# Kernel tuning notes

Hardware: AMD Instinct MI355X
Metric: run time of the kernel (lower is better)

The kernel has to match this reference:

```python
import jax, jax.numpy as jnp
from jax import lax
import numpy as np

NUM_CLASSES = 10
NUM_ITERS = 3


def conv2d(x, w, stride):
    return lax.conv_general_dilated(x, w, window_strides=stride, padding='VALID',
                                    dimension_numbers=('NCHW', 'OIHW', 'NCHW'))


def deconv(x, w_torch, stride, pad):
    # w_torch: [Cin, Cout, k, k] (PyTorch ConvTranspose2d layout)
    k = w_torch.shape[2]
    w = jnp.flip(w_torch, axis=(2, 3)).transpose(1, 0, 2, 3)  # -> [Cout, Cin, k, k]
    return lax.conv_general_dilated(x, w, window_strides=(1, 1),
                                    padding=[(k - 1 - pad, k - 1 - pad)] * 2,
                                    lhs_dilation=(stride, stride),
                                    dimension_numbers=('NCHW', 'OIHW', 'NCHW'))


def squash(t, axis=-1):
    sq = jnp.sum(t * t, axis=axis, keepdims=True)
    return (sq / (1.0 + sq)) * t / jnp.sqrt(sq)


def batchnorm(t, g, b, eps=1e-5):
    # training-mode batch statistics over (N, H, W)
    m = t.mean(axis=(0, 2, 3), keepdims=True)
    v = t.var(axis=(0, 2, 3), keepdims=True)
    return g[None, :, None, None] * (t - m) / jnp.sqrt(v + eps) + b[None, :, None, None]


def setup_inputs() -> dict:
    key = jax.random.key(0)
    ks = jax.random.split(key, 16)
    B = 128
    d = dict(
        x=jax.random.normal(ks[0], (B, 3, 32, 32), jnp.float32),
        conv1_w=jax.random.normal(ks[1], (256, 3, 9, 9), jnp.float32) * 0.05,
        conv1_b=jnp.zeros((256,), jnp.float32),
        prim_w=jax.random.normal(ks[2], (8, 64, 256, 9, 9), jnp.float32) * 0.02,
        prim_b=jnp.zeros((8, 64), jnp.float32),
        route_w=jax.random.normal(ks[3], (NUM_CLASSES, 4096, 8, 16), jnp.float32),
        g1_w=jax.random.normal(ks[4], (160, 256, 4, 4), jnp.float32) * 0.02,
        g2_w=jax.random.normal(ks[5], (256, 128, 4, 4), jnp.float32) * 0.02,
        g3_w=jax.random.normal(ks[6], (128, 64, 4, 4), jnp.float32) * 0.02,
        g4_w=jax.random.normal(ks[7], (64, 3, 4, 4), jnp.float32) * 0.02,
        bn1_g=jnp.ones((256,), jnp.float32), bn1_b=jnp.zeros((256,), jnp.float32),
        bn2_g=jnp.ones((128,), jnp.float32), bn2_b=jnp.zeros((128,), jnp.float32),
        bn3_g=jnp.ones((64,), jnp.float32), bn3_b=jnp.zeros((64,), jnp.float32),
    )
    return d


def reference(x, conv1_w, conv1_b, prim_w, prim_b, route_w,
              g1_w, g2_w, g3_w, g4_w,
              bn1_g, bn1_b, bn2_g, bn2_b, bn3_g, bn3_b):
    B = x.shape[0]
    # conv stem: [B,3,32,32] -> [B,256,24,24]
    h = jax.nn.relu(conv2d(x, conv1_w, (1, 1)) + conv1_b[None, :, None, None])
    # primary capsules: 8 parallel convs fused into one [8*64,256,9,9] conv -> [B,512,8,8]
    u = conv2d(h, prim_w.reshape(8 * 64, 256, 9, 9), (2, 2)) + prim_b.reshape(8 * 64)[None, :, None, None]
    # cat over capsules on last dim: route node = flat (c,h,w) per capsule -> [B,4096,8]
    u = u.reshape(B, 8, 64 * 8 * 8).transpose(0, 2, 1)
    u = squash(u, axis=-1)
    # digit capsules: priors [C,B,R,16]
    priors = jnp.einsum('bri,crio->cbro', u, route_w)
    logits = jnp.zeros(priors.shape[:3], priors.dtype)  # [C,B,R]
    v = None
    for i in range(NUM_ITERS):
        probs = jax.nn.softmax(logits, axis=2)  # over route nodes (dim=2 in original)
        v = squash(jnp.einsum('cbr,cbro->cbo', probs, priors), axis=-1)  # [C,B,16]
        if i != NUM_ITERS - 1:
            logits = logits + jnp.einsum('cbro,cbo->cbr', priors, v)
    caps = v.transpose(1, 0, 2)  # [B,10,16]
    classes = jax.nn.softmax(jnp.sqrt(jnp.sum(caps * caps, axis=-1)), axis=-1)  # [B,10]
    # y = one-hot of predicted class (inference path, y=None)
    y = jax.nn.one_hot(jnp.argmax(classes, axis=1), NUM_CLASSES, dtype=caps.dtype)
    z = (caps * y[:, :, None]).reshape(B, 160, 1, 1)
    # DCGAN generator: 1 -> 4 -> 8 -> 16 -> 32
    t = jax.nn.relu(batchnorm(deconv(z, g1_w, 1, 0), bn1_g, bn1_b))
    t = jax.nn.relu(batchnorm(deconv(t, g2_w, 2, 1), bn2_g, bn2_b))
    t = jax.nn.relu(batchnorm(deconv(t, g3_w, 2, 1), bn3_g, bn3_b))
    recon = jnp.tanh(deconv(t, g4_w, 2, 1))  # [B,3,32,32]
    return classes, recon
```

## Files before the change

kernel.cpp:

```cpp
#include <hip/hip_runtime.h>
#include <cmath>

#define NB 128

#define H_STRIDE 600
#define W_SLAB   7776

__global__ __launch_bounds__(192) void conv1_kernel(
    const float* __restrict__ x, const float* __restrict__ w,
    const float* __restrict__ bias, float* __restrict__ h)
{
    __shared__ float4 xs4[768];
    float* xs = (float*)xs4;
    int b = blockIdx.x, cobase = blockIdx.y * 8, tid = threadIdx.x;
    const float4* xsrc = (const float4*)(x + (size_t)b * 3072);
    for (int i = tid; i < 768; i += 192) xs4[i] = xsrc[i];
    __syncthreads();
    for (int round = 0; round < 3; ++round) {
        int px = round * 192 + tid;
        int yy = px / 24, xx = px - yy * 24;
        float acc[8];
        #pragma unroll
        for (int cc = 0; cc < 8; ++cc) acc[cc] = 0.f;
        for (int c = 0; c < 3; ++c)
            for (int ky = 0; ky < 9; ++ky) {
                const float* xr = xs + c * 1024 + (yy + ky) * 32 + xx;
                float xv[9];
                #pragma unroll
                for (int kx = 0; kx < 9; ++kx) xv[kx] = xr[kx];
                int tb = c * 81 + ky * 9;
                #pragma unroll
                for (int cc = 0; cc < 8; ++cc) {
                    const float* wp = w + (cobase + cc) * 243 + tb;
                    #pragma unroll
                    for (int kx = 0; kx < 9; ++kx) acc[cc] += xv[kx] * wp[kx];
                }
            }
        #pragma unroll
        for (int cc = 0; cc < 8; ++cc)
            h[((size_t)b * 256 + cobase + cc) * H_STRIDE + yy * 25 + xx] =
                fmaxf(acc[cc] + bias[cobase + cc], 0.f);
    }
}

__global__ __launch_bounds__(128) void primw_transpose_kernel(
    const float* __restrict__ pw, float* __restrict__ wt)
{
    int g = blockIdx.x >> 8, ci = blockIdx.x & 255;
    int half = threadIdx.x >> 6, lane = threadIdx.x & 63;
    for (int ch = half; ch < 64; ch += 2) {
        int oct = ch >> 3, k = ch & 7;
        const float* src = pw + ((size_t)(g * 64 + ch) * 256 + ci) * 81;
        float* dst = wt + (size_t)(g * 256 + ci) * W_SLAB + oct * 12 + k;
        dst[(size_t)lane * 96] = src[lane];
        if (lane < 17) dst[(size_t)(64 + lane) * 96] = src[64 + lane];
    }
}

__global__ __launch_bounds__(256) void prim_conv_kernel(
    const float* __restrict__ h, const float* __restrict__ wt,
    float* __restrict__ part)
{
    __shared__ __align__(16) float wsh[W_SLAB];
    __shared__ __align__(16) float hsh[2 * H_STRIDE];
    int b2 = blockIdx.x, g = blockIdx.y, half = blockIdx.z, tid = threadIdx.x;
    int ci0 = half * 128;
    int img = tid >> 7;
    int t128 = tid & 127;
    int oct = t128 & 7;
    int pq = t128 >> 3;
    int px0 = pq * 4;
    int y0 = pq >> 1, x0 = (pq & 1) * 4;
    int b = b2 * 2 + img;
    int hbase = img * H_STRIDE;

    float acc[8][4];
    #pragma unroll
    for (int i = 0; i < 8; ++i)
        #pragma unroll
        for (int j = 0; j < 4; ++j) acc[i][j] = 0.f;

    #define STAGE(ci)                                                                        \
    {                                                                                        \
        const float* wsrc = wt + (size_t)(g * 256 + (ci)) * W_SLAB;                          \
        const float* h0src = h + ((size_t)(b2 * 2 + 0) * 256 + (ci)) * H_STRIDE;             \
        const float* h1src = h + ((size_t)(b2 * 2 + 1) * 256 + (ci)) * H_STRIDE;             \
        _Pragma("unroll")                                                                    \
        for (int k = 0; k < 7; ++k)                                                          \
            __builtin_amdgcn_global_load_lds(                                                \
                (const unsigned int*)wsrc + (k * 256 + tid) * 4,                             \
                (unsigned int*)wsh + (k * 256 + tid) * 4, 16, 0, 0);                         \
        if (tid < 152)                                                                       \
            __builtin_amdgcn_global_load_lds(                                                \
                (const unsigned int*)wsrc + (1792 + tid) * 4,                                \
                (unsigned int*)wsh + (1792 + tid) * 4, 16, 0, 0);                            \
        if (tid < 150)                                                                       \
            __builtin_amdgcn_global_load_lds(                                                \
                (const unsigned int*)h0src + tid * 4,                                        \
                (unsigned int*)hsh + tid * 4, 16, 0, 0);                                     \
        if (tid < 150)                                                                       \
            __builtin_amdgcn_global_load_lds(                                                \
                (const unsigned int*)h1src + tid * 4,                                        \
                (unsigned int*)(hsh + H_STRIDE) + tid * 4, 16, 0, 0);                        \
    }

    STAGE(ci0);
    asm volatile("s_waitcnt vmcnt(0)" ::: "memory");
    __syncthreads();

    for (int ci = ci0; ci < ci0 + 128; ++ci) {
        #pragma unroll 3
        for (int ky = 0; ky < 9; ++ky) {
            int hrowbase = hbase + (2 * y0 + ky) * 25 + 2 * x0;
            #pragma unroll
            for (int kx = 0; kx < 9; ++kx) {
                const float* wp = wsh + (ky * 9 + kx) * 96 + oct * 12;
                float4 wa = *(const float4*)(wp);
                float4 wb = *(const float4*)(wp + 4);
                int hr = hrowbase + kx;
                float h0 = hsh[hr];
                float h1 = hsh[hr + 2];
                float h2 = hsh[hr + 4];
                float h3 = hsh[hr + 6];
                float wv[8] = {wa.x, wa.y, wa.z, wa.w, wb.x, wb.y, wb.z, wb.w};
                #pragma unroll
                for (int i = 0; i < 8; ++i) {
                    acc[i][0] += wv[i] * h0;
                    acc[i][1] += wv[i] * h1;
                    acc[i][2] += wv[i] * h2;
                    acc[i][3] += wv[i] * h3;
                }
            }
        }
        __syncthreads();
        if (ci + 1 < ci0 + 128) STAGE(ci + 1);
        asm volatile("s_waitcnt vmcnt(0)" ::: "memory");
        __syncthreads();
    }
    #undef STAGE

    float* pp = part + ((size_t)(half * 128 + b) * 8 + g) * 4096;
    #pragma unroll
    for (int i = 0; i < 8; ++i) {
        int c64 = oct * 8 + i;
        *(float4*)(pp + c64 * 64 + px0) =
            make_float4(acc[i][0], acc[i][1], acc[i][2], acc[i][3]);
    }
}

__global__ void squash_u_kernel(const float* __restrict__ part,
                                const float* __restrict__ pb, float* __restrict__ ut)
{
    int b = blockIdx.x; int r = blockIdx.y * 256 + threadIdx.x;
    int c64 = r >> 6;
    const float* p0 = part + (size_t)b * 8 * 4096 + r;
    const float* p1 = part + (size_t)(128 + b) * 8 * 4096 + r;
    float v[8]; float sq = 0.f;
    #pragma unroll
    for (int i = 0; i < 8; ++i) {
        v[i] = p0[(size_t)i * 4096] + p1[(size_t)i * 4096] + pb[i * 64 + c64];
        sq += v[i] * v[i];
    }
    float sc = sqrtf(sq) / (1.f + sq);
    float4 o0 = make_float4(v[0] * sc, v[1] * sc, v[2] * sc, v[3] * sc);
    float4 o1 = make_float4(v[4] * sc, v[5] * sc, v[6] * sc, v[7] * sc);
    float* o = ut + ((size_t)b * 4096 + r) * 8;
    *(float4*)o = o0; *(float4*)(o + 4) = o1;
}

__global__ void softmax_stats_kernel(const float* __restrict__ logits,
                                     float* __restrict__ mbuf, float* __restrict__ sebuf)
{
    int cb = blockIdx.x; int tid = threadIdx.x;
    const float* lrow = logits + (size_t)cb * 4096;
    float mx = -1e30f;
    for (int i = tid; i < 4096; i += 256) mx = fmaxf(mx, lrow[i]);
    #pragma unroll
    for (int d = 1; d < 64; d <<= 1) mx = fmaxf(mx, __shfl_xor(mx, d));
    __shared__ float rm[4], rs[4];
    if ((tid & 63) == 0) rm[tid >> 6] = mx;
    __syncthreads();
    mx = fmaxf(fmaxf(rm[0], rm[1]), fmaxf(rm[2], rm[3]));
    float s = 0.f;
    for (int i = tid; i < 4096; i += 256) s += expf(lrow[i] - mx);
    #pragma unroll
    for (int d = 1; d < 64; d <<= 1) s += __shfl_xor(s, d);
    if ((tid & 63) == 0) rs[tid >> 6] = s;
    __syncthreads();
    if (tid == 0) {
        mbuf[cb] = mx;
        sebuf[cb] = rs[0] + rs[1] + rs[2] + rs[3];
    }
}

__global__ __launch_bounds__(256) void route_s_kernel(
    const float* __restrict__ logits, const float* __restrict__ ut,
    const float* __restrict__ route_w, const float* __restrict__ mbuf,
    const float* __restrict__ sebuf, float* __restrict__ spart)
{
    __shared__ __align__(16) float smem[11232];
    const int UB = 4224, PB = 8400, RB = 8928;
    int c = blockIdx.x, ch = blockIdx.y, tid = threadIdx.x;
    int r0 = ch * 32;

    {
        const float4* w4 = (const float4*)(route_w + ((size_t)c * 4096 + r0) * 128);
        #pragma unroll
        for (int k = 0; k < 4; ++k) {
            int idx = k * 256 + tid;
            float4 wv = w4[idx];
            int rl = idx >> 5, rem = (idx & 31) * 4;
            *(float4*)(smem + rl * 132 + rem) = wv;
        }
    }

    int bC = tid & 15, igC = (tid >> 4) & 7, ohC = tid >> 7;

    for (int bg = 0; bg < 8; ++bg) {
        int b0 = bg * 16;
        __syncthreads();
        {
            int bb = tid >> 4, seg = tid & 15;
            const float4* us = (const float4*)(ut + (size_t)(b0 + bb) * 32768 + (size_t)r0 * 8);
            #pragma unroll
            for (int q = 0; q < 4; ++q) {
                float4 v = us[seg * 4 + q];
                int base = UB + bb * 261 + (seg * 4 + q) * 4;
                smem[base + 0] = v.x; smem[base + 1] = v.y;
                smem[base + 2] = v.z; smem[base + 3] = v.w;
            }
        }
        if (tid < 128) {
            int b = tid >> 3, rr = tid & 7;
            int cb = c * 128 + b0 + b;
            float m = mbuf[cb];
            float inv = 1.0f / sebuf[cb];
            float4 lv = *(const float4*)(logits + (size_t)cb * 4096 + r0 + rr * 4);
            int pbb = PB + b * 33 + rr * 4;
            smem[pbb + 0] = expf(lv.x - m) * inv;
            smem[pbb + 1] = expf(lv.y - m) * inv;
            smem[pbb + 2] = expf(lv.z - m) * inv;
            smem[pbb + 3] = expf(lv.w - m) * inv;
        }
        __syncthreads();
        float4 a0 = make_float4(0.f, 0.f, 0.f, 0.f);
        float4 a1 = make_float4(0.f, 0.f, 0.f, 0.f);
        int ub = UB + bC * 261 + igC;
        int wb = igC * 16 + ohC * 8;
        int pbb = PB + bC * 33;
        for (int rl = 0; rl < 32; ++rl) {
            float uu = smem[ub + rl * 8];
            float pr = smem[pbb + rl];
            float t1 = pr * uu;
            const float* wp = smem + rl * 132 + wb;
            float4 w0 = *(const float4*)wp;
            float4 w1 = *(const float4*)(wp + 4);
            a0.x += t1 * w0.x; a0.y += t1 * w0.y; a0.z += t1 * w0.z; a0.w += t1 * w0.w;
            a1.x += t1 * w1.x; a1.y += t1 * w1.y; a1.z += t1 * w1.z; a1.w += t1 * w1.w;
        }
        int rb = RB + tid * 9;
        smem[rb + 0] = a0.x; smem[rb + 1] = a0.y; smem[rb + 2] = a0.z; smem[rb + 3] = a0.w;
        smem[rb + 4] = a1.x; smem[rb + 5] = a1.y; smem[rb + 6] = a1.z; smem[rb + 7] = a1.w;
        __syncthreads();
        {
            int o = tid & 15, b = tid >> 4;
            int oh = o >> 3, ol = o & 7;
            float s = 0.f;
            #pragma unroll
            for (int ig = 0; ig < 8; ++ig)
                s += smem[RB + (b + 16 * ig + 128 * oh) * 9 + ol];
            spart[(size_t)ch * 20480 + (size_t)(c * 128 + b0 + b) * 16 + o] = s;
        }
    }
}

__global__ void route_v_kernel(const float* __restrict__ spart, float* __restrict__ vbuf)
{
    int cb = blockIdx.x * 64 + threadIdx.x;
    float4 a0 = make_float4(0,0,0,0), a1 = make_float4(0,0,0,0);
    float4 a2 = make_float4(0,0,0,0), a3 = make_float4(0,0,0,0);
    for (int k = 0; k < 128; ++k) {
        const float4* p = (const float4*)(spart + (size_t)k * 20480 + (size_t)cb * 16);
        float4 b0 = p[0], b1 = p[1], b2 = p[2], b3 = p[3];
        a0.x += b0.x; a0.y += b0.y; a0.z += b0.z; a0.w += b0.w;
        a1.x += b1.x; a1.y += b1.y; a1.z += b1.z; a1.w += b1.w;
        a2.x += b2.x; a2.y += b2.y; a2.z += b2.z; a2.w += b2.w;
        a3.x += b3.x; a3.y += b3.y; a3.z += b3.z; a3.w += b3.w;
    }
    float sq = a0.x*a0.x + a0.y*a0.y + a0.z*a0.z + a0.w*a0.w
             + a1.x*a1.x + a1.y*a1.y + a1.z*a1.z + a1.w*a1.w
             + a2.x*a2.x + a2.y*a2.y + a2.z*a2.z + a2.w*a2.w
             + a3.x*a3.x + a3.y*a3.y + a3.z*a3.z + a3.w*a3.w;
    float sc = sqrtf(sq) / (1.f + sq);
    float4* vp = (float4*)(vbuf + (size_t)cb * 16);
    vp[0] = make_float4(a0.x*sc, a0.y*sc, a0.z*sc, a0.w*sc);
    vp[1] = make_float4(a1.x*sc, a1.y*sc, a1.z*sc, a1.w*sc);
    vp[2] = make_float4(a2.x*sc, a2.y*sc, a2.z*sc, a2.w*sc);
    vp[3] = make_float4(a3.x*sc, a3.y*sc, a3.z*sc, a3.w*sc);
}

__global__ __launch_bounds__(256) void route_upd_kernel(
    float* __restrict__ logits, const float* __restrict__ ut,
    const float* __restrict__ route_w, const float* __restrict__ vbuf)
{
    __shared__ __align__(16) float smem[8400];
    const int UB = 4224;
    int c = blockIdx.x, ch = blockIdx.y, tid = threadIdx.x;
    int r0 = ch * 32;
    {
        const float4* w4 = (const float4*)(route_w + ((size_t)c * 4096 + r0) * 128);
        #pragma unroll
        for (int k = 0; k < 4; ++k) {
            int idx = k * 256 + tid;
            float4 wv = w4[idx];
            int rl = idx >> 5, rem = (idx & 31) * 4;
            *(float4*)(smem + rl * 132 + rem) = wv;
        }
    }
    int b = tid & 15, rg = tid >> 4;
    for (int bg = 0; bg < 8; ++bg) {
        int b0 = bg * 16;
        __syncthreads();
        {
            int bb = tid >> 4, seg = tid & 15;
            const float4* us = (const float4*)(ut + (size_t)(b0 + bb) * 32768 + (size_t)r0 * 8);
            #pragma unroll
            for (int q = 0; q < 4; ++q) {
                float4 v = us[seg * 4 + q];
                int base = UB + bb * 261 + (seg * 4 + q) * 4;
                smem[base + 0] = v.x; smem[base + 1] = v.y;
                smem[base + 2] = v.z; smem[base + 3] = v.w;
            }
        }
        __syncthreads();
        int cb = c * 128 + b0 + b;
        const float4* vp = (const float4*)(vbuf + (size_t)cb * 16);
        float4 v0 = vp[0], v1 = vp[1], v2 = vp[2], v3 = vp[3];
        #pragma unroll
        for (int jj = 0; jj < 2; ++jj) {
            int rl = rg * 2 + jj;
            float4 p0 = make_float4(0,0,0,0), p1 = make_float4(0,0,0,0);
            float4 p2 = make_float4(0,0,0,0), p3 = make_float4(0,0,0,0);
            int ub = UB + b * 261 + rl * 8;
            #pragma unroll
            for (int i = 0; i < 8; ++i) {
                float uu = smem[ub + i];
                const float* wp = smem + rl * 132 + i * 16;
                float4 w0 = *(const float4*)wp;
                float4 w1 = *(const float4*)(wp + 4);
                float4 w2 = *(const float4*)(wp + 8);
                float4 w3 = *(const float4*)(wp + 12);
                p0.x += uu*w0.x; p0.y += uu*w0.y; p0.z += uu*w0.z; p0.w += uu*w0.w;
                p1.x += uu*w1.x; p1.y += uu*w1.y; p1.z += uu*w1.z; p1.w += uu*w1.w;
                p2.x += uu*w2.x; p2.y += uu*w2.y; p2.z += uu*w2.z; p2.w += uu*w2.w;
                p3.x += uu*w3.x; p3.y += uu*w3.y; p3.z += uu*w3.z; p3.w += uu*w3.w;
            }
            float delta = p0.x*v0.x + p0.y*v0.y + p0.z*v0.z + p0.w*v0.w
                        + p1.x*v1.x + p1.y*v1.y + p1.z*v1.z + p1.w*v1.w
                        + p2.x*v2.x + p2.y*v2.y + p2.z*v2.z + p2.w*v2.w
                        + p3.x*v3.x + p3.y*v3.y + p3.z*v3.z + p3.w*v3.w;
            logits[(size_t)cb * 4096 + r0 + rl] += delta;
        }
    }
}

__global__ void caps_out_kernel(const float* __restrict__ vbuf,
                                float* __restrict__ out_classes, float* __restrict__ zbuf)
{
    int b = threadIdx.x;
    float norms[10];
    #pragma unroll
    for (int c = 0; c < 10; ++c) {
        const float* vp = vbuf + (size_t)(c * 128 + b) * 16;
        float sq = 0.f;
        #pragma unroll
        for (int o = 0; o < 16; ++o) sq += vp[o] * vp[o];
        norms[c] = sqrtf(sq);
    }
    float mx = norms[0]; int am = 0;
    #pragma unroll
    for (int c = 1; c < 10; ++c) if (norms[c] > mx) { mx = norms[c]; am = c; }
    float se = 0.f; float e[10];
    #pragma unroll
    for (int c = 0; c < 10; ++c) { e[c] = expf(norms[c] - mx); se += e[c]; }
    float isd = 1.f / se;
    #pragma unroll
    for (int c = 0; c < 10; ++c) out_classes[b * 10 + c] = e[c] * isd;
    #pragma unroll
    for (int c = 0; c < 10; ++c) {
        const float* vp = vbuf + (size_t)(c * 128 + b) * 16;
        #pragma unroll
        for (int o = 0; o < 16; ++o)
            zbuf[b * 160 + c * 16 + o] = (c == am) ? vp[o] : 0.f;
    }
}

__global__ void gen1_kernel(const float* __restrict__ z, const float* __restrict__ w,
                            float* __restrict__ out)
{
    int idx = blockIdx.x * 256 + threadIdx.x;
    int j = idx & 4095; int b = idx >> 12;
    const float* zp = z + b * 160;
    float a = 0.f;
    #pragma unroll 4
    for (int ci = 0; ci < 160; ++ci) a += zp[ci] * w[(size_t)ci * 4096 + j];
    out[idx] = a;
}

template <int C, int HW>
__global__ void bn_stats_kernel(const float* __restrict__ t, const float* __restrict__ g,
                                const float* __restrict__ beta,
                                float* __restrict__ scale, float* __restrict__ shift)
{
    int co = blockIdx.x; int tid = threadIdx.x;
    float s = 0.f, s2 = 0.f;
    for (int i = tid; i < NB * HW; i += 256) {
        int b = i / HW, hw = i - b * HW;
        float v = t[((size_t)b * C + co) * HW + hw];
        s += v; s2 += v * v;
    }
    #pragma unroll
    for (int d = 1; d < 64; d <<= 1) { s += __shfl_xor(s, d); s2 += __shfl_xor(s2, d); }
    __shared__ float rs[4], rs2[4];
    if ((tid & 63) == 0) { rs[tid >> 6] = s; rs2[tid >> 6] = s2; }
    __syncthreads();
    if (tid == 0) {
        float S = rs[0] + rs[1] + rs[2] + rs[3];
        float S2 = rs2[0] + rs2[1] + rs2[2] + rs2[3];
        const float n = (float)(NB * HW);
        float mean = S / n;
        float var = S2 / n - mean * mean;
        float r = 1.f / sqrtf(var + 1e-5f);
        scale[co] = g[co] * r;
        shift[co] = beta[co] - mean * g[co] * r;
    }
}

template <int C, int HW>
__global__ void bn_apply_kernel(float* __restrict__ t, const float* __restrict__ scale,
                                const float* __restrict__ shift, int total)
{
    int idx = blockIdx.x * 256 + threadIdx.x;
    if (idx < total) {
        int co = (idx / HW) % C;
        t[idx] = fmaxf(t[idx] * scale[co] + shift[co], 0.f);
    }
}

template <int Ci, int Co, int S, int SPLIT>
__global__ __launch_bounds__(256) void deconv_row_kernel(
    const float* __restrict__ in, const float* __restrict__ w,
    float* __restrict__ out)
{
    constexpr int OS = 2 * S;
    constexpr int ROWS = Co * OS;
    constexpr int RPB = ROWS / SPLIT;
    __shared__ __align__(16) float ish[Ci * S * S];
    int b = blockIdx.x, rb = blockIdx.y, tid = threadIdx.x;
    const float4* src = (const float4*)(in + (size_t)b * Ci * S * S);
    for (int i = tid; i < Ci * S * S / 4; i += 256) ((float4*)ish)[i] = src[i];
    __syncthreads();

    for (int r = rb * RPB + tid; r < (rb + 1) * RPB; r += 256) {
        int co = r / OS, oy = r % OS;
        float acc[OS];
        #pragma unroll
        for (int j = 0; j < OS; ++j) acc[j] = 0.f;
        int p = (oy + 1) & 1;
        for (int ci = 0; ci < Ci; ++ci) {
            const float* wci = w + ((size_t)ci * Co + co) * 16;
            #pragma unroll
            for (int t = 0; t < 2; ++t) {
                int ky = p + 2 * t;
                int iy = (oy + 1 - ky) >> 1;
                if (iy < 0 || iy >= S) continue;
                float4 wv = *(const float4*)(wci + ky * 4);
                const float* irow = ish + (ci * S + iy) * S;
                #pragma unroll
                for (int ox = 0; ox < OS; ++ox) {
                    int q = (ox + 1) & 1;
                    int ix0 = (ox + 1 - q) >> 1;
                    int ix1 = ix0 - 1;
                    float wk0 = q ? wv.y : wv.x;
                    float wk2 = q ? wv.w : wv.z;
                    if (ix0 < S)  acc[ox] += wk0 * irow[ix0];
                    if (ix1 >= 0) acc[ox] += wk2 * irow[ix1];
                }
            }
        }
        float* orow = out + ((size_t)(b * Co + co) * OS + oy) * OS;
        #pragma unroll
        for (int j = 0; j < OS; j += 4)
            *(float4*)(orow + j) = make_float4(acc[j], acc[j+1], acc[j+2], acc[j+3]);
    }
}

template <int Ci, int Co, int S, bool TANH>
__global__ void deconv_kernel(const float* __restrict__ in, const float* __restrict__ w,
                              float* __restrict__ out)
{
    constexpr int OS = 2 * S;
    int idx = blockIdx.x * 256 + threadIdx.x;
    int ox = idx % OS; int t = idx / OS;
    int oy = t % OS; int t2 = t / OS;
    int co = t2 % Co; int b = t2 / Co;
    float a = 0.f;
    #pragma unroll
    for (int ky = 0; ky < 4; ++ky) {
        int ty = oy + 1 - ky;
        if (ty & 1) continue;
        int iy = ty >> 1;
        if (iy < 0 || iy >= S) continue;
        #pragma unroll
        for (int kx = 0; kx < 4; ++kx) {
            int tx = ox + 1 - kx;
            if (tx & 1) continue;
            int ix = tx >> 1;
            if (ix < 0 || ix >= S) continue;
            const float* ip = in + ((size_t)b * Ci * S + iy) * S + ix;
            const float* wp = w + co * 16 + ky * 4 + kx;
            #pragma unroll 4
            for (int ci = 0; ci < Ci; ++ci)
                a += ip[(size_t)ci * S * S] * wp[(size_t)ci * Co * 16];
        }
    }
    out[idx] = TANH ? tanhf(a) : a;
}

extern "C" void kernel_launch(void* const* d_in, const int* in_sizes, int n_in,
                              void* d_out, int out_size, void* d_ws, size_t ws_size,
                              hipStream_t stream)
{
    const float* x       = (const float*)d_in[0];
    const float* conv1_w = (const float*)d_in[1];
    const float* conv1_b = (const float*)d_in[2];
    const float* prim_w  = (const float*)d_in[3];
    const float* prim_b  = (const float*)d_in[4];
    const float* route_w = (const float*)d_in[5];
    const float* g1_w    = (const float*)d_in[6];
    const float* g2_w    = (const float*)d_in[7];
    const float* g3_w    = (const float*)d_in[8];
    const float* g4_w    = (const float*)d_in[9];
    const float* bn1_g   = (const float*)d_in[10];
    const float* bn1_b   = (const float*)d_in[11];
    const float* bn2_g   = (const float*)d_in[12];
    const float* bn2_b   = (const float*)d_in[13];
    const float* bn3_g   = (const float*)d_in[14];
    const float* bn3_b   = (const float*)d_in[15];
    float* outf = (float*)d_out;

    float* ws = (float*)d_ws;
    float* h      = ws;
    float* wt     = h + 19660800;
    float* part   = wt + 15925248;
    float* logits = wt;
    float* ut     = wt + 5242880;
    float* mbuf   = part;
    float* sebuf  = part + 1280;
    float* vbuf   = part + 2560;
    float* zbuf   = part + 23040;
    float* bnsc   = part + 64000;
    float* t1b    = part + 64896;
    float* t2b    = part + 589184;
    float* t3b    = part + 1637760;
    float* spart  = part + 4194304;

    primw_transpose_kernel<<<dim3(2048), 128, 0, stream>>>(prim_w, wt);
    conv1_kernel<<<dim3(128, 32), 192, 0, stream>>>(x, conv1_w, conv1_b, h);
    prim_conv_kernel<<<dim3(64, 8, 2), 256, 0, stream>>>(h, wt, part);
    squash_u_kernel<<<dim3(128, 16), 256, 0, stream>>>(part, prim_b, ut);

    hipMemsetAsync(logits, 0, (size_t)5242880 * sizeof(float), stream);
    for (int it = 0; it < 3; ++it) {
        softmax_stats_kernel<<<dim3(1280), 256, 0, stream>>>(logits, mbuf, sebuf);
        route_s_kernel<<<dim3(10, 128), 256, 0, stream>>>(logits, ut, route_w, mbuf, sebuf, spart);
        route_v_kernel<<<dim3(20), 64, 0, stream>>>(spart, vbuf);
        if (it < 2)
            route_upd_kernel<<<dim3(10, 128), 256, 0, stream>>>(logits, ut, route_w, vbuf);
    }
    caps_out_kernel<<<dim3(1), 128, 0, stream>>>(vbuf, outf, zbuf);

    gen1_kernel<<<dim3(2048), 256, 0, stream>>>(zbuf, g1_w, t1b);
    bn_stats_kernel<256, 16><<<dim3(256), 256, 0, stream>>>(t1b, bn1_g, bn1_b, bnsc, bnsc + 256);
    bn_apply_kernel<256, 16><<<dim3(2048), 256, 0, stream>>>(t1b, bnsc, bnsc + 256, 524288);

    deconv_row_kernel<256, 128, 4, 4><<<dim3(128, 4), 256, 0, stream>>>(t1b, g2_w, t2b);
    bn_stats_kernel<128, 64><<<dim3(128), 256, 0, stream>>>(t2b, bn2_g, bn2_b, bnsc + 512, bnsc + 640);
    bn_apply_kernel<128, 64><<<dim3(4096), 256, 0, stream>>>(t2b, bnsc + 512, bnsc + 640, 1048576);

    deconv_row_kernel<128, 64, 8, 4><<<dim3(128, 4), 256, 0, stream>>>(t2b, g3_w, t3b);
    bn_stats_kernel<64, 256><<<dim3(64), 256, 0, stream>>>(t3b, bn3_g, bn3_b, bnsc + 768, bnsc + 832);
    bn_apply_kernel<64, 256><<<dim3(8192), 256, 0, stream>>>(t3b, bnsc + 768, bnsc + 832, 2097152);

    deconv_kernel<64, 3, 16, true><<<dim3(1536), 256, 0, stream>>>(t3b, g4_w, outf + 1280);
}
```

Before: 4.031 ms.

## Retile primary-capsule conv to 4 channels by 8 pixels per thread with register row cache

```diff
diff --git a/kernel.cpp b/kernel.cpp
--- a/kernel.cpp
+++ b/kernel.cpp
@@ -46,14 +46,19 @@
 __global__ __launch_bounds__(128) void primw_transpose_kernel(
     const float* __restrict__ pw, float* __restrict__ wt)
 {
-    int g = blockIdx.x >> 8, ci = blockIdx.x & 255;
-    int half = threadIdx.x >> 6, lane = threadIdx.x & 63;
-    for (int ch = half; ch < 64; ch += 2) {
-        int oct = ch >> 3, k = ch & 7;
-        const float* src = pw + ((size_t)(g * 64 + ch) * 256 + ci) * 81;
-        float* dst = wt + (size_t)(g * 256 + ci) * W_SLAB + oct * 12 + k;
-        dst[(size_t)lane * 96] = src[lane];
-        if (lane < 17) dst[(size_t)(64 + lane) * 96] = src[64 + lane];
+    __shared__ float buf[64 * 82];
+    int g = blockIdx.x >> 8, ci = blockIdx.x & 255, tid = threadIdx.x;
+    for (int idx = tid; idx < 5184; idx += 128) {
+        int ch = idx / 81, t = idx - ch * 81;
+        buf[ch * 82 + t] = pw[((size_t)(g * 64 + ch) * 256 + ci) * 81 + t];
+    }
+    __syncthreads();
+    float* dst = wt + (size_t)(g * 256 + ci) * W_SLAB;
+    for (int f = tid; f < W_SLAB; f += 128) {
+        int tap = f / 96;
+        int rem = f - tap * 96;
+        int oct = rem / 12, k = rem - oct * 12;
+        dst[f] = (k < 8) ? buf[(oct * 8 + k) * 82 + tap] : 0.f;
     }
 }
 
@@ -67,18 +72,17 @@
     int ci0 = half * 128;
     int img = tid >> 7;
     int t128 = tid & 127;
-    int oct = t128 & 7;
-    int pq = t128 >> 3;
-    int px0 = pq * 4;
-    int y0 = pq >> 1, x0 = (pq & 1) * 4;
+    int quad = t128 & 15;
+    int prow = t128 >> 4;
     int b = b2 * 2 + img;
     int hbase = img * H_STRIDE;
-
-    float acc[8][4];
-    #pragma unroll
-    for (int i = 0; i < 8; ++i)
-        #pragma unroll
-        for (int j = 0; j < 4; ++j) acc[i][j] = 0.f;
+    int woff = (quad >> 1) * 12 + (quad & 1) * 4;
+
+    float acc[4][8];
+    #pragma unroll
+    for (int i = 0; i < 4; ++i)
+        #pragma unroll
+        for (int j = 0; j < 8; ++j) acc[i][j] = 0.f;
 
     #define STAGE(ci)                                                                        \
     {                                                                                        \
@@ -111,24 +115,20 @@
     for (int ci = ci0; ci < ci0 + 128; ++ci) {
         #pragma unroll 3
         for (int ky = 0; ky < 9; ++ky) {
-            int hrowbase = hbase + (2 * y0 + ky) * 25 + 2 * x0;
+            int hr = hbase + (2 * prow + ky) * 25;
+            float hv[23];
+            #pragma unroll
+            for (int t = 0; t < 23; ++t) hv[t] = hsh[hr + t];
             #pragma unroll
             for (int kx = 0; kx < 9; ++kx) {
-                const float* wp = wsh + (ky * 9 + kx) * 96 + oct * 12;
-                float4 wa = *(const float4*)(wp);
-                float4 wb = *(const float4*)(wp + 4);
-                int hr = hrowbase + kx;
-                float h0 = hsh[hr];
-                float h1 = hsh[hr + 2];
-                float h2 = hsh[hr + 4];
-                float h3 = hsh[hr + 6];
-                float wv[8] = {wa.x, wa.y, wa.z, wa.w, wb.x, wb.y, wb.z, wb.w};
+                const float* wp = wsh + (ky * 9 + kx) * 96 + woff;
+                float4 wa = *(const float4*)wp;
+                float wv[4] = {wa.x, wa.y, wa.z, wa.w};
                 #pragma unroll
-                for (int i = 0; i < 8; ++i) {
-                    acc[i][0] += wv[i] * h0;
-                    acc[i][1] += wv[i] * h1;
-                    acc[i][2] += wv[i] * h2;
-                    acc[i][3] += wv[i] * h3;
+                for (int j = 0; j < 8; ++j) {
+                    float hx = hv[2 * j + kx];
+                    #pragma unroll
+                    for (int i = 0; i < 4; ++i) acc[i][j] += wv[i] * hx;
                 }
             }
         }
@@ -141,10 +141,12 @@
 
     float* pp = part + ((size_t)(half * 128 + b) * 8 + g) * 4096;
     #pragma unroll
-    for (int i = 0; i < 8; ++i) {
-        int c64 = oct * 8 + i;
-        *(float4*)(pp + c64 * 64 + px0) =
+    for (int i = 0; i < 4; ++i) {
+        int c64 = quad * 4 + i;
+        *(float4*)(pp + c64 * 64 + prow * 8) =
             make_float4(acc[i][0], acc[i][1], acc[i][2], acc[i][3]);
+        *(float4*)(pp + c64 * 64 + prow * 8 + 4) =
+            make_float4(acc[i][4], acc[i][5], acc[i][6], acc[i][7]);
     }
 }
 
```

Measured after the change: 4.193 ms. +4.0%, slower.
